# Performance work log

Hardware: AMD Instinct MI355X
Metric: run time of the kernel (lower is better)

## Reference

```python
import jax, jax.numpy as jnp
import numpy as np

N, K, D = 32768, 32, 64
LOG_2PI = float(np.log(2.0 * np.pi))


def setup_inputs() -> dict:
    key = jax.random.key(0)
    k1, k2, k3, k4 = jax.random.split(key, 4)
    X = jax.random.normal(k1, (N, D), dtype=jnp.float32)
    mu = jax.random.normal(k2, (K, D), dtype=jnp.float32)
    L = jax.random.normal(k3, (K, D, D), dtype=jnp.float32) * 0.1
    weights = jax.random.normal(k4, (K,), dtype=jnp.float32)
    return {"X": X, "mu": mu, "L": L, "weights": weights, "it": 0}


def reference(X, mu, L, weights, it):
    d = X.shape[1]
    # Cholesky composition: Sigma_k = tril(L_k) @ tril(L_k).T + I  (always PD)
    Lt = jnp.tril(L)                                   # [K, D, D]
    sigmas = Lt @ jnp.swapaxes(Lt, -1, -2) + jnp.eye(d, dtype=X.dtype)
    _, logdet = jnp.linalg.slogdet(sigmas)             # [K] (det > 0, sign = +1)
    Sinv = jnp.linalg.inv(sigmas)                      # [K, D, D]
    # Batched squared Mahalanobis distance: [N, K]
    diff = X[:, None, :] - mu[None, :, :]              # [N, K, D]
    maha = jnp.einsum("nkd,kde,nke->nk", diff, Sinv, diff)
    log_w = jax.nn.log_softmax(weights)                # [K]
    # log component density + log mixture weight
    logp = -0.5 * (d * LOG_2PI + logdet[None, :] + maha) + log_w[None, :]
    # pdf = sum_k exp(logp); log_likelihood = log(pdf)  (stable via logsumexp)
    loglik = jax.scipy.special.logsumexp(logp, axis=1)  # [N]
    # forward = -log_likelihoods(X).logsumexp(dim=0)
    return -jax.scipy.special.logsumexp(loglik, axis=0)
```

## Files before the change

kernel.cpp:

```cpp
#include <hip/hip_runtime.h>
#include <math.h>

#define DIM 64
#define KC 32
#define NPTS 32768
#define LOG_2PI 1.8378770664093453f
#define C0 (-58.0f)
#define ST 68

typedef __attribute__((ext_vector_type(8))) short short8;
typedef __attribute__((ext_vector_type(4))) float float4v;

__device__ __forceinline__ unsigned short f2bf(float f) {
    unsigned u = __float_as_uint(f);
    u += 0x7FFFu + ((u >> 16) & 1u);
    return (unsigned short)(u >> 16);
}

__device__ __forceinline__ float rdlane(float v, int l) {
    return __int_as_float(__builtin_amdgcn_readlane(__float_as_int(v), l));
}

template <int CTRL>
__device__ __forceinline__ float dpp_add(float x) {
    int t = __builtin_amdgcn_mov_dpp(__float_as_int(x), CTRL, 0xF, 0xF, true);
    return x + __int_as_float(t);
}
__device__ __forceinline__ float sum16(float x) {
    x = dpp_add<0xB1>(x);
    x = dpp_add<0x4E>(x);
    x = dpp_add<0x141>(x);
    x = dpp_add<0x140>(x);
    return x;
}

__global__ __launch_bounds__(256) void prep_kernel(
    const float* __restrict__ L, const float* __restrict__ mu,
    const float* __restrict__ w, short* __restrict__ Bpack,
    float* __restrict__ cstC)
{
    const int k = blockIdx.x;
    const int t = threadIdx.x;
    const int wv = t >> 6;
    const int ln = t & 63;
    __shared__ float Llds[DIM * ST];
    __shared__ float Sig[DIM * ST];
    __shared__ float Clds[DIM * ST];
    __shared__ float Ylds[DIM * ST];
    __shared__ float qlds[DIM];
    __shared__ float rdbuf[DIM];
    __shared__ float ldet;

    for (int idx = t; idx < DIM * DIM; idx += 256) {
        int r = idx >> 6, c = idx & 63;
        float v = L[(size_t)k * DIM * DIM + idx];
        Llds[r * ST + c] = (c <= r) ? v : 0.f;
    }
    for (int idx = t; idx < DIM * ST; idx += 256) {
        Clds[idx] = 0.f;
        Ylds[idx] = 0.f;
    }
    __syncthreads();

    {
        float Lr[DIM];
        const float2* lp = (const float2*)(Llds + ln * ST);
#pragma unroll
        for (int p = 0; p < 32; ++p) {
            float2 v = lp[p];
            Lr[2 * p] = v.x; Lr[2 * p + 1] = v.y;
        }
#pragma unroll 1
        for (int jj = 0; jj < 16; ++jj) {
            const int j = wv * 16 + jj;
            const float2* up = (const float2*)(Llds + j * ST);
            float a0 = 0.f, a1 = 0.f, a2 = 0.f, a3 = 0.f;
#pragma unroll
            for (int p = 0; p < 32; p += 2) {
                float2 u0 = up[p], u1 = up[p + 1];
                a0 = fmaf(Lr[2 * p], u0.x, a0);
                a1 = fmaf(Lr[2 * p + 1], u0.y, a1);
                a2 = fmaf(Lr[2 * p + 2], u1.x, a2);
                a3 = fmaf(Lr[2 * p + 3], u1.y, a3);
            }
            float s = (a0 + a1) + (a2 + a3);
            if (j == ln) s += 1.f;
            Sig[ln * ST + j] = s;
        }
    }
    __syncthreads();

    {
        const float2* crow = (const float2*)(Clds + ln * ST);
        const float2* yrow = (const float2*)(Ylds + ln * ST);
        float ld2 = 0.f;
#pragma unroll 1
        for (int c = 0; c < DIM; c += 4) {
            const float2* u0 = (const float2*)(Clds + (c + 0) * ST);
            const float2* u1 = (const float2*)(Clds + (c + 1) * ST);
            const float2* u2 = (const float2*)(Clds + (c + 2) * ST);
            const float2* u3 = (const float2*)(Clds + (c + 3) * ST);
            float si0 = 0.f, si1 = 0.f, si2 = 0.f, si3 = 0.f;
            if (wv == 0) {
                float d0a = 0.f, d0b = 0.f, d1a = 0.f, d1b = 0.f;
                float d2a = 0.f, d2b = 0.f, d3a = 0.f, d3b = 0.f;
#pragma unroll
                for (int p = 0; p < 32; ++p) {
                    float2 cr = crow[p];
                    float2 a0 = u0[p], a1 = u1[p], a2 = u2[p], a3 = u3[p];
                    d0a = fmaf(cr.x, a0.x, d0a); d0b = fmaf(cr.y, a0.y, d0b);
                    d1a = fmaf(cr.x, a1.x, d1a); d1b = fmaf(cr.y, a1.y, d1b);
                    d2a = fmaf(cr.x, a2.x, d2a); d2b = fmaf(cr.y, a2.y, d2b);
                    d3a = fmaf(cr.x, a3.x, d3a); d3b = fmaf(cr.y, a3.y, d3b);
                }
                const float4 sg = *(const float4*)(Sig + ln * ST + c);
                float s0 = sg.x - (d0a + d0b);
                float s1 = sg.y - (d1a + d1b);
                float s2 = sg.z - (d2a + d2b);
                float s3 = sg.w - (d3a + d3b);
                float dd0 = rdlane(s0, c + 0);
                float rd0 = __builtin_amdgcn_rsqf(dd0);
                float c0v = s0 * rd0;
                s1 = fmaf(-c0v, rdlane(c0v, c + 1), s1);
                s2 = fmaf(-c0v, rdlane(c0v, c + 2), s2);
                s3 = fmaf(-c0v, rdlane(c0v, c + 3), s3);
                float dd1 = rdlane(s1, c + 1);
                float rd1 = __builtin_amdgcn_rsqf(dd1);
                float c1v = s1 * rd1;
                s2 = fmaf(-c1v, rdlane(c1v, c + 2), s2);
                s3 = fmaf(-c1v, rdlane(c1v, c + 3), s3);
                float dd2 = rdlane(s2, c + 2);
                float rd2 = __builtin_amdgcn_rsqf(dd2);
                float c2v = s2 * rd2;
                s3 = fmaf(-c2v, rdlane(c2v, c + 3), s3);
                float dd3 = rdlane(s3, c + 3);
                float rd3 = __builtin_amdgcn_rsqf(dd3);
                float c3v = s3 * rd3;
                ld2 += (__logf(dd0) + __logf(dd1)) + (__logf(dd2) + __logf(dd3));
                *(float4*)(Clds + ln * ST + c) = make_float4(c0v, c1v, c2v, c3v);
                if (ln == 0) *(float4*)(rdbuf + c) = make_float4(rd0, rd1, rd2, rd3);
            } else if (wv == 1) {
                float e0a = 0.f, e0b = 0.f, e1a = 0.f, e1b = 0.f;
                float e2a = 0.f, e2b = 0.f, e3a = 0.f, e3b = 0.f;
#pragma unroll
                for (int p = 0; p < 32; ++p) {
                    float2 yr = yrow[p];
                    float2 a0 = u0[p], a1 = u1[p], a2 = u2[p], a3 = u3[p];
                    e0a = fmaf(yr.x, a0.x, e0a); e0b = fmaf(yr.y, a0.y, e0b);
                    e1a = fmaf(yr.x, a1.x, e1a); e1b = fmaf(yr.y, a1.y, e1b);
                    e2a = fmaf(yr.x, a2.x, e2a); e2b = fmaf(yr.y, a2.y, e2b);
                    e3a = fmaf(yr.x, a3.x, e3a); e3b = fmaf(yr.y, a3.y, e3b);
                }
                si0 = ((ln == c + 0) ? 1.f : 0.f) - (e0a + e0b);
                si1 = ((ln == c + 1) ? 1.f : 0.f) - (e1a + e1b);
                si2 = ((ln == c + 2) ? 1.f : 0.f) - (e2a + e2b);
                si3 = ((ln == c + 3) ? 1.f : 0.f) - (e3a + e3b);
            }
            __syncthreads();
            if (wv == 1) {
                const float4 rdv = *(const float4*)(rdbuf + c);
                float C10 = Clds[(c + 1) * ST + c];
                float C20 = Clds[(c + 2) * ST + c];
                float C21 = Clds[(c + 2) * ST + c + 1];
                float C30 = Clds[(c + 3) * ST + c];
                float C31 = Clds[(c + 3) * ST + c + 1];
                float C32 = Clds[(c + 3) * ST + c + 2];
                float y0 = si0 * rdv.x;
                float y1 = (si1 - C10 * y0) * rdv.y;
                float y2 = (si2 - C20 * y0 - C21 * y1) * rdv.z;
                float y3 = (si3 - C30 * y0 - C31 * y1 - C32 * y2) * rdv.w;
                float4 yo;
                yo.x = (ln <= c + 0) ? y0 : 0.f;
                yo.y = (ln <= c + 1) ? y1 : 0.f;
                yo.z = (ln <= c + 2) ? y2 : 0.f;
                yo.w = (ln <= c + 3) ? y3 : 0.f;
                *(float4*)(Ylds + ln * ST + c) = yo;
            }
        }
        if (wv == 0 && ln == 0) ldet = ld2;
    }
    __syncthreads();

    if (wv == 0) {
        const float* muk = mu + k * DIM;
        float qv = 0.f;
#pragma unroll 8
        for (int j = 0; j < DIM; ++j)
            qv = fmaf(Ylds[j * ST + ln], muk[j], qv);
        qlds[ln] = qv;
        if (ln == 0) {
            float wm = -3.0e38f;
            for (int i = 0; i < KC; ++i) wm = fmaxf(wm, w[i]);
            float se = 0.f;
            for (int i = 0; i < KC; ++i) se += __expf(w[i] - wm);
            float logw = w[k] - (wm + __logf(se));
            cstC[k] = -0.5f * (DIM * LOG_2PI + ldet) + logw - C0;
        }
    }
    __syncthreads();

    {
        const int ct = wv;
        const int col = ct * 16 + (ln & 15);
        const int kb = (ln >> 4) * 8;
#pragma unroll
        for (int kt = 0; kt < 3; ++kt) {
            short8 v;
            if (kt < 2) {
#pragma unroll
                for (int e = 0; e < 8; ++e)
                    v[e] = (short)f2bf(Ylds[(kt * 32 + kb + e) * ST + col]);
            } else {
#pragma unroll
                for (int e = 0; e < 8; ++e)
                    v[e] = (short)((kb + e == 0) ? f2bf(-qlds[col]) : 0);
            }
            *(short8*)(Bpack + ((size_t)(k * 12 + ct * 3 + kt) * 64 + ln) * 8) = v;
        }
    }
}

__global__ __launch_bounds__(256, 2) void main_kernel(
    const float* __restrict__ X, const float* __restrict__ Bpack,
    const float* __restrict__ cstC, float* __restrict__ partials)
{
    const int tid = threadIdx.x;
    const int lane = tid & 63;
    const int wv = tid >> 6;
    const int ks = blockIdx.x & 7;
    const int g = blockIdx.x >> 3;
    const int m = lane & 15;

    __shared__ float4 Bsh[3072];
    {
        const float4* Bg = (const float4*)Bpack + (size_t)ks * 3072;
#pragma unroll
        for (int it = 0; it < 12; ++it)
            Bsh[it * 256 + tid] = Bg[it * 256 + tid];
    }

    const int rbase = g * 128 + wv * 32;
    const int jb = (lane >> 4) * 8;
    const float* Xr0 = X + (size_t)(rbase + m) * DIM;
    const float* Xr1 = Xr0 + 16 * DIM;
    short8 a0, a1, b0r, b1r;
#pragma unroll
    for (int e = 0; e < 8; ++e) {
        a0[e] = (short)f2bf(Xr0[jb + e]);
        a1[e] = (short)f2bf(Xr0[32 + jb + e]);
        b0r[e] = (short)f2bf(Xr1[jb + e]);
        b1r[e] = (short)f2bf(Xr1[32 + jb + e]);
    }

    __syncthreads();

    const short8* Bs = (const short8*)Bsh;
    const short* Bss = (const short*)Bsh;
    float acc = 0.f;
#pragma unroll
    for (int kk = 0; kk < 4; ++kk) {
        const int k = ks * 4 + kk;
        float p0 = 0.f, p1 = 0.f, p2 = 0.f, p3 = 0.f;
        float r0 = 0.f, r1 = 0.f, r2 = 0.f, r3 = 0.f;
#pragma unroll
        for (int ct = 0; ct < 4; ++ct) {
            short8 f0 = Bs[(kk * 12 + ct * 3 + 0) * 64 + lane];
            short8 f1 = Bs[(kk * 12 + ct * 3 + 1) * 64 + lane];
            short nqs = Bss[(size_t)((kk * 12 + ct * 3 + 2) * 64 + m) * 8];
            float nq = __int_as_float(((int)(unsigned short)nqs) << 16);
            float4v c0 = {nq, nq, nq, nq};
            c0 = __builtin_amdgcn_mfma_f32_16x16x32_bf16(a0, f0, c0, 0, 0, 0);
            c0 = __builtin_amdgcn_mfma_f32_16x16x32_bf16(a1, f1, c0, 0, 0, 0);
            float4v c1 = {nq, nq, nq, nq};
            c1 = __builtin_amdgcn_mfma_f32_16x16x32_bf16(b0r, f0, c1, 0, 0, 0);
            c1 = __builtin_amdgcn_mfma_f32_16x16x32_bf16(b1r, f1, c1, 0, 0, 0);
            p0 = fmaf(c0[0], c0[0], p0); p1 = fmaf(c0[1], c0[1], p1);
            p2 = fmaf(c0[2], c0[2], p2); p3 = fmaf(c0[3], c0[3], p3);
            r0 = fmaf(c1[0], c1[0], r0); r1 = fmaf(c1[1], c1[1], r1);
            r2 = fmaf(c1[2], c1[2], r2); r3 = fmaf(c1[3], c1[3], r3);
        }
        const float cc = cstC[k];
        acc += __expf(fmaf(-0.5f, sum16(p0), cc)) + __expf(fmaf(-0.5f, sum16(p1), cc));
        acc += __expf(fmaf(-0.5f, sum16(p2), cc)) + __expf(fmaf(-0.5f, sum16(p3), cc));
        acc += __expf(fmaf(-0.5f, sum16(r0), cc)) + __expf(fmaf(-0.5f, sum16(r1), cc));
        acc += __expf(fmaf(-0.5f, sum16(r2), cc)) + __expf(fmaf(-0.5f, sum16(r3), cc));
    }
    acc += __shfl_xor(acc, 16, 64);
    acc += __shfl_xor(acc, 32, 64);

    __shared__ float pm[4];
    if (lane == 0) pm[wv] = acc;
    __syncthreads();
    if (tid == 0)
        partials[blockIdx.x] = (pm[0] + pm[1]) + (pm[2] + pm[3]);
}

__global__ __launch_bounds__(256) void final_kernel(
    const float* __restrict__ partials, int n, float* __restrict__ out)
{
    const int tid = threadIdx.x;
    float s = 0.f;
    for (int i = tid; i < n; i += 256) s += partials[i];
#pragma unroll
    for (int mm = 1; mm <= 32; mm <<= 1) s += __shfl_xor(s, mm, 64);
    __shared__ float pm[4];
    if ((tid & 63) == 0) pm[tid >> 6] = s;
    __syncthreads();
    if (tid == 0) out[0] = -(C0 + logf((pm[0] + pm[1]) + (pm[2] + pm[3])));
}

extern "C" void kernel_launch(void* const* d_in, const int* in_sizes, int n_in,
                              void* d_out, int out_size, void* d_ws, size_t ws_size,
                              hipStream_t stream) {
    const float* X  = (const float*)d_in[0];
    const float* mu = (const float*)d_in[1];
    const float* L  = (const float*)d_in[2];
    const float* w  = (const float*)d_in[3];

    char* ws = (char*)d_ws;
    short* Bpack = (short*)ws;
    float* cstC  = (float*)(ws + 32 * 12 * 64 * 8 * 2);
    float* parts = cstC + KC;

    prep_kernel<<<KC, 256, 0, stream>>>(L, mu, w, Bpack, cstC);
    main_kernel<<<2048, 256, 0, stream>>>(X, (const float*)Bpack, cstC, parts);
    final_kernel<<<1, 256, 0, stream>>>(parts, 2048, (float*)d_out);
}
```

Baseline: 113.3 us.

## Fuse prep, main and final reduction into one kernel with flag sync

Merges the per-component Cholesky/inverse prep, the MFMA Mahalanobis main pass and the final logsumexp into a single launch. The first 32 blocks do the prep work and publish ready flags; every block loads its X fragment first, then spins on the flags before staging the packed B matrices. The last block to finish, found through an atomic counter, performs the final reduction. This removes two kernel launches and lets X loads overlap the prep. The risks: the flags are never reset between calls, so later calls can read Bpack while it is being rewritten. Also, the larger shared-memory union and the spin-wait depend on the prep blocks being resident first.

```diff
diff --git a/kernel.cpp b/kernel.cpp
--- a/kernel.cpp
+++ b/kernel.cpp
@@ -7,6 +7,7 @@
 #define LOG_2PI 1.8378770664093453f
 #define C0 (-58.0f)
 #define ST 68
+#define MAGIC 0x13579BDF
 
 typedef __attribute__((ext_vector_type(8))) short short8;
 typedef __attribute__((ext_vector_type(4))) float float4v;
@@ -34,210 +35,221 @@
     return x;
 }
 
-__global__ __launch_bounds__(256) void prep_kernel(
-    const float* __restrict__ L, const float* __restrict__ mu,
-    const float* __restrict__ w, short* __restrict__ Bpack,
-    float* __restrict__ cstC)
+struct PrepSh {
+    float Llds[DIM * ST];
+    float Sig[DIM * ST];
+    float Clds[DIM * ST];
+    float Ylds[DIM * ST];
+    float qlds[DIM];
+    float rdbuf[DIM];
+    float ldet;
+};
+struct MainSh {
+    float4 Bsh[3072];
+    float pm[4];
+};
+union SharedU { PrepSh p; MainSh m; };
+
+__global__ __launch_bounds__(256, 2) void fused_kernel(
+    const float* __restrict__ X, const float* __restrict__ mu,
+    const float* __restrict__ L, const float* __restrict__ w,
+    short* __restrict__ Bpack, float* __restrict__ cstC,
+    float* __restrict__ partials, int* __restrict__ flags,
+    int* __restrict__ tailctr, float* __restrict__ out)
 {
-    const int k = blockIdx.x;
-    const int t = threadIdx.x;
-    const int wv = t >> 6;
-    const int ln = t & 63;
-    __shared__ float Llds[DIM * ST];
-    __shared__ float Sig[DIM * ST];
-    __shared__ float Clds[DIM * ST];
-    __shared__ float Ylds[DIM * ST];
-    __shared__ float qlds[DIM];
-    __shared__ float rdbuf[DIM];
-    __shared__ float ldet;
-
-    for (int idx = t; idx < DIM * DIM; idx += 256) {
-        int r = idx >> 6, c = idx & 63;
-        float v = L[(size_t)k * DIM * DIM + idx];
-        Llds[r * ST + c] = (c <= r) ? v : 0.f;
-    }
-    for (int idx = t; idx < DIM * ST; idx += 256) {
-        Clds[idx] = 0.f;
-        Ylds[idx] = 0.f;
-    }
-    __syncthreads();
-
-    {
-        float Lr[DIM];
-        const float2* lp = (const float2*)(Llds + ln * ST);
-#pragma unroll
-        for (int p = 0; p < 32; ++p) {
-            float2 v = lp[p];
-            Lr[2 * p] = v.x; Lr[2 * p + 1] = v.y;
-        }
-#pragma unroll 1
-        for (int jj = 0; jj < 16; ++jj) {
-            const int j = wv * 16 + jj;
-            const float2* up = (const float2*)(Llds + j * ST);
-            float a0 = 0.f, a1 = 0.f, a2 = 0.f, a3 = 0.f;
-#pragma unroll
-            for (int p = 0; p < 32; p += 2) {
-                float2 u0 = up[p], u1 = up[p + 1];
-                a0 = fmaf(Lr[2 * p], u0.x, a0);
-                a1 = fmaf(Lr[2 * p + 1], u0.y, a1);
-                a2 = fmaf(Lr[2 * p + 2], u1.x, a2);
-                a3 = fmaf(Lr[2 * p + 3], u1.y, a3);
-            }
-            float s = (a0 + a1) + (a2 + a3);
-            if (j == ln) s += 1.f;
-            Sig[ln * ST + j] = s;
-        }
-    }
-    __syncthreads();
-
-    {
-        const float2* crow = (const float2*)(Clds + ln * ST);
-        const float2* yrow = (const float2*)(Ylds + ln * ST);
-        float ld2 = 0.f;
-#pragma unroll 1
-        for (int c = 0; c < DIM; c += 4) {
-            const float2* u0 = (const float2*)(Clds + (c + 0) * ST);
-            const float2* u1 = (const float2*)(Clds + (c + 1) * ST);
-            const float2* u2 = (const float2*)(Clds + (c + 2) * ST);
-            const float2* u3 = (const float2*)(Clds + (c + 3) * ST);
-            float si0 = 0.f, si1 = 0.f, si2 = 0.f, si3 = 0.f;
-            if (wv == 0) {
-                float d0a = 0.f, d0b = 0.f, d1a = 0.f, d1b = 0.f;
-                float d2a = 0.f, d2b = 0.f, d3a = 0.f, d3b = 0.f;
-#pragma unroll
-                for (int p = 0; p < 32; ++p) {
-                    float2 cr = crow[p];
-                    float2 a0 = u0[p], a1 = u1[p], a2 = u2[p], a3 = u3[p];
-                    d0a = fmaf(cr.x, a0.x, d0a); d0b = fmaf(cr.y, a0.y, d0b);
-                    d1a = fmaf(cr.x, a1.x, d1a); d1b = fmaf(cr.y, a1.y, d1b);
-                    d2a = fmaf(cr.x, a2.x, d2a); d2b = fmaf(cr.y, a2.y, d2b);
-                    d3a = fmaf(cr.x, a3.x, d3a); d3b = fmaf(cr.y, a3.y, d3b);
-                }
-                const float4 sg = *(const float4*)(Sig + ln * ST + c);
-                float s0 = sg.x - (d0a + d0b);
-                float s1 = sg.y - (d1a + d1b);
-                float s2 = sg.z - (d2a + d2b);
-                float s3 = sg.w - (d3a + d3b);
-                float dd0 = rdlane(s0, c + 0);
-                float rd0 = __builtin_amdgcn_rsqf(dd0);
-                float c0v = s0 * rd0;
-                s1 = fmaf(-c0v, rdlane(c0v, c + 1), s1);
-                s2 = fmaf(-c0v, rdlane(c0v, c + 2), s2);
-                s3 = fmaf(-c0v, rdlane(c0v, c + 3), s3);
-                float dd1 = rdlane(s1, c + 1);
-                float rd1 = __builtin_amdgcn_rsqf(dd1);
-                float c1v = s1 * rd1;
-                s2 = fmaf(-c1v, rdlane(c1v, c + 2), s2);
-                s3 = fmaf(-c1v, rdlane(c1v, c + 3), s3);
-                float dd2 = rdlane(s2, c + 2);
-                float rd2 = __builtin_amdgcn_rsqf(dd2);
-                float c2v = s2 * rd2;
-                s3 = fmaf(-c2v, rdlane(c2v, c + 3), s3);
-                float dd3 = rdlane(s3, c + 3);
-                float rd3 = __builtin_amdgcn_rsqf(dd3);
-                float c3v = s3 * rd3;
-                ld2 += (__logf(dd0) + __logf(dd1)) + (__logf(dd2) + __logf(dd3));
-                *(float4*)(Clds + ln * ST + c) = make_float4(c0v, c1v, c2v, c3v);
-                if (ln == 0) *(float4*)(rdbuf + c) = make_float4(rd0, rd1, rd2, rd3);
-            } else if (wv == 1) {
-                float e0a = 0.f, e0b = 0.f, e1a = 0.f, e1b = 0.f;
-                float e2a = 0.f, e2b = 0.f, e3a = 0.f, e3b = 0.f;
-#pragma unroll
-                for (int p = 0; p < 32; ++p) {
-                    float2 yr = yrow[p];
-                    float2 a0 = u0[p], a1 = u1[p], a2 = u2[p], a3 = u3[p];
-                    e0a = fmaf(yr.x, a0.x, e0a); e0b = fmaf(yr.y, a0.y, e0b);
-                    e1a = fmaf(yr.x, a1.x, e1a); e1b = fmaf(yr.y, a1.y, e1b);
-                    e2a = fmaf(yr.x, a2.x, e2a); e2b = fmaf(yr.y, a2.y, e2b);
-                    e3a = fmaf(yr.x, a3.x, e3a); e3b = fmaf(yr.y, a3.y, e3b);
-                }
-                si0 = ((ln == c + 0) ? 1.f : 0.f) - (e0a + e0b);
-                si1 = ((ln == c + 1) ? 1.f : 0.f) - (e1a + e1b);
-                si2 = ((ln == c + 2) ? 1.f : 0.f) - (e2a + e2b);
-                si3 = ((ln == c + 3) ? 1.f : 0.f) - (e3a + e3b);
-            }
-            __syncthreads();
-            if (wv == 1) {
-                const float4 rdv = *(const float4*)(rdbuf + c);
-                float C10 = Clds[(c + 1) * ST + c];
-                float C20 = Clds[(c + 2) * ST + c];
-                float C21 = Clds[(c + 2) * ST + c + 1];
-                float C30 = Clds[(c + 3) * ST + c];
-                float C31 = Clds[(c + 3) * ST + c + 1];
-                float C32 = Clds[(c + 3) * ST + c + 2];
-                float y0 = si0 * rdv.x;
-                float y1 = (si1 - C10 * y0) * rdv.y;
-                float y2 = (si2 - C20 * y0 - C21 * y1) * rdv.z;
-                float y3 = (si3 - C30 * y0 - C31 * y1 - C32 * y2) * rdv.w;
-                float4 yo;
-                yo.x = (ln <= c + 0) ? y0 : 0.f;
-                yo.y = (ln <= c + 1) ? y1 : 0.f;
-                yo.z = (ln <= c + 2) ? y2 : 0.f;
-                yo.w = (ln <= c + 3) ? y3 : 0.f;
-                *(float4*)(Ylds + ln * ST + c) = yo;
-            }
-        }
-        if (wv == 0 && ln == 0) ldet = ld2;
-    }
-    __syncthreads();
-
-    if (wv == 0) {
-        const float* muk = mu + k * DIM;
-        float qv = 0.f;
-#pragma unroll 8
-        for (int j = 0; j < DIM; ++j)
-            qv = fmaf(Ylds[j * ST + ln], muk[j], qv);
-        qlds[ln] = qv;
-        if (ln == 0) {
-            float wm = -3.0e38f;
-            for (int i = 0; i < KC; ++i) wm = fmaxf(wm, w[i]);
-            float se = 0.f;
-            for (int i = 0; i < KC; ++i) se += __expf(w[i] - wm);
-            float logw = w[k] - (wm + __logf(se));
-            cstC[k] = -0.5f * (DIM * LOG_2PI + ldet) + logw - C0;
-        }
-    }
-    __syncthreads();
-
-    {
-        const int ct = wv;
-        const int col = ct * 16 + (ln & 15);
-        const int kb = (ln >> 4) * 8;
-#pragma unroll
-        for (int kt = 0; kt < 3; ++kt) {
-            short8 v;
-            if (kt < 2) {
-#pragma unroll
-                for (int e = 0; e < 8; ++e)
-                    v[e] = (short)f2bf(Ylds[(kt * 32 + kb + e) * ST + col]);
-            } else {
-#pragma unroll
-                for (int e = 0; e < 8; ++e)
-                    v[e] = (short)((kb + e == 0) ? f2bf(-qlds[col]) : 0);
-            }
-            *(short8*)(Bpack + ((size_t)(k * 12 + ct * 3 + kt) * 64 + ln) * 8) = v;
-        }
-    }
-}
-
-__global__ __launch_bounds__(256, 2) void main_kernel(
-    const float* __restrict__ X, const float* __restrict__ Bpack,
-    const float* __restrict__ cstC, float* __restrict__ partials)
-{
+    const int bid = blockIdx.x;
     const int tid = threadIdx.x;
     const int lane = tid & 63;
     const int wv = tid >> 6;
-    const int ks = blockIdx.x & 7;
-    const int g = blockIdx.x >> 3;
+    __shared__ SharedU sh;
+    __shared__ int lastdone;
+
+    if (bid == 0 && tid == 0) *tailctr = 0;
+
+    if (bid < KC) {
+        const int k = bid;
+        const int t = tid;
+        const int ln = lane;
+        float* Llds = sh.p.Llds;
+        float* Sig  = sh.p.Sig;
+        float* Clds = sh.p.Clds;
+        float* Ylds = sh.p.Ylds;
+
+        for (int idx = t; idx < DIM * DIM; idx += 256) {
+            int r = idx >> 6, c = idx & 63;
+            float v = L[(size_t)k * DIM * DIM + idx];
+            Llds[r * ST + c] = (c <= r) ? v : 0.f;
+        }
+        for (int idx = t; idx < DIM * ST; idx += 256) {
+            Clds[idx] = 0.f;
+            Ylds[idx] = 0.f;
+        }
+        __syncthreads();
+
+        {
+            float Lr[DIM];
+            const float2* lp = (const float2*)(Llds + ln * ST);
+#pragma unroll
+            for (int p = 0; p < 32; ++p) {
+                float2 v = lp[p];
+                Lr[2 * p] = v.x; Lr[2 * p + 1] = v.y;
+            }
+#pragma unroll 1
+            for (int jj = 0; jj < 16; ++jj) {
+                const int j = wv * 16 + jj;
+                const float2* up = (const float2*)(Llds + j * ST);
+                float a0 = 0.f, a1 = 0.f, a2 = 0.f, a3 = 0.f;
+#pragma unroll
+                for (int p = 0; p < 32; p += 2) {
+                    float2 u0 = up[p], u1 = up[p + 1];
+                    a0 = fmaf(Lr[2 * p], u0.x, a0);
+                    a1 = fmaf(Lr[2 * p + 1], u0.y, a1);
+                    a2 = fmaf(Lr[2 * p + 2], u1.x, a2);
+                    a3 = fmaf(Lr[2 * p + 3], u1.y, a3);
+                }
+                float s = (a0 + a1) + (a2 + a3);
+                if (j == ln) s += 1.f;
+                Sig[ln * ST + j] = s;
+            }
+        }
+        __syncthreads();
+
+        {
+            const float2* crow = (const float2*)(Clds + ln * ST);
+            const float2* yrow = (const float2*)(Ylds + ln * ST);
+            float ld2 = 0.f;
+#pragma unroll 1
+            for (int c = 0; c < DIM; c += 4) {
+                const float2* u0 = (const float2*)(Clds + (c + 0) * ST);
+                const float2* u1 = (const float2*)(Clds + (c + 1) * ST);
+                const float2* u2 = (const float2*)(Clds + (c + 2) * ST);
+                const float2* u3 = (const float2*)(Clds + (c + 3) * ST);
+                float si0 = 0.f, si1 = 0.f, si2 = 0.f, si3 = 0.f;
+                if (wv == 0) {
+                    float d0a = 0.f, d0b = 0.f, d1a = 0.f, d1b = 0.f;
+                    float d2a = 0.f, d2b = 0.f, d3a = 0.f, d3b = 0.f;
+#pragma unroll
+                    for (int p = 0; p < 32; ++p) {
+                        float2 cr = crow[p];
+                        float2 a0 = u0[p], a1 = u1[p], a2 = u2[p], a3 = u3[p];
+                        d0a = fmaf(cr.x, a0.x, d0a); d0b = fmaf(cr.y, a0.y, d0b);
+                        d1a = fmaf(cr.x, a1.x, d1a); d1b = fmaf(cr.y, a1.y, d1b);
+                        d2a = fmaf(cr.x, a2.x, d2a); d2b = fmaf(cr.y, a2.y, d2b);
+                        d3a = fmaf(cr.x, a3.x, d3a); d3b = fmaf(cr.y, a3.y, d3b);
+                    }
+                    const float4 sg = *(const float4*)(Sig + ln * ST + c);
+                    float s0 = sg.x - (d0a + d0b);
+                    float s1 = sg.y - (d1a + d1b);
+                    float s2 = sg.z - (d2a + d2b);
+                    float s3 = sg.w - (d3a + d3b);
+                    float dd0 = rdlane(s0, c + 0);
+                    float rd0 = __builtin_amdgcn_rsqf(dd0);
+                    float c0v = s0 * rd0;
+                    s1 = fmaf(-c0v, rdlane(c0v, c + 1), s1);
+                    s2 = fmaf(-c0v, rdlane(c0v, c + 2), s2);
+                    s3 = fmaf(-c0v, rdlane(c0v, c + 3), s3);
+                    float dd1 = rdlane(s1, c + 1);
+                    float rd1 = __builtin_amdgcn_rsqf(dd1);
+                    float c1v = s1 * rd1;
+                    s2 = fmaf(-c1v, rdlane(c1v, c + 2), s2);
+                    s3 = fmaf(-c1v, rdlane(c1v, c + 3), s3);
+                    float dd2 = rdlane(s2, c + 2);
+                    float rd2 = __builtin_amdgcn_rsqf(dd2);
+                    float c2v = s2 * rd2;
+                    s3 = fmaf(-c2v, rdlane(c2v, c + 3), s3);
+                    float dd3 = rdlane(s3, c + 3);
+                    float rd3 = __builtin_amdgcn_rsqf(dd3);
+                    float c3v = s3 * rd3;
+                    ld2 += (__logf(dd0) + __logf(dd1)) + (__logf(dd2) + __logf(dd3));
+                    *(float4*)(Clds + ln * ST + c) = make_float4(c0v, c1v, c2v, c3v);
+                    if (ln == 0) *(float4*)(sh.p.rdbuf + c) = make_float4(rd0, rd1, rd2, rd3);
+                } else if (wv == 1) {
+                    float e0a = 0.f, e0b = 0.f, e1a = 0.f, e1b = 0.f;
+                    float e2a = 0.f, e2b = 0.f, e3a = 0.f, e3b = 0.f;
+#pragma unroll
+                    for (int p = 0; p < 32; ++p) {
+                        float2 yr = yrow[p];
+                        float2 a0 = u0[p], a1 = u1[p], a2 = u2[p], a3 = u3[p];
+                        e0a = fmaf(yr.x, a0.x, e0a); e0b = fmaf(yr.y, a0.y, e0b);
+                        e1a = fmaf(yr.x, a1.x, e1a); e1b = fmaf(yr.y, a1.y, e1b);
+                        e2a = fmaf(yr.x, a2.x, e2a); e2b = fmaf(yr.y, a2.y, e2b);
+                        e3a = fmaf(yr.x, a3.x, e3a); e3b = fmaf(yr.y, a3.y, e3b);
+                    }
+                    si0 = ((ln == c + 0) ? 1.f : 0.f) - (e0a + e0b);
+                    si1 = ((ln == c + 1) ? 1.f : 0.f) - (e1a + e1b);
+                    si2 = ((ln == c + 2) ? 1.f : 0.f) - (e2a + e2b);
+                    si3 = ((ln == c + 3) ? 1.f : 0.f) - (e3a + e3b);
+                }
+                __syncthreads();
+                if (wv == 1) {
+                    const float4 rdv = *(const float4*)(sh.p.rdbuf + c);
+                    float C10 = Clds[(c + 1) * ST + c];
+                    float C20 = Clds[(c + 2) * ST + c];
+                    float C21 = Clds[(c + 2) * ST + c + 1];
+                    float C30 = Clds[(c + 3) * ST + c];
+                    float C31 = Clds[(c + 3) * ST + c + 1];
+                    float C32 = Clds[(c + 3) * ST + c + 2];
+                    float y0 = si0 * rdv.x;
+                    float y1 = (si1 - C10 * y0) * rdv.y;
+                    float y2 = (si2 - C20 * y0 - C21 * y1) * rdv.z;
+                    float y3 = (si3 - C30 * y0 - C31 * y1 - C32 * y2) * rdv.w;
+                    float4 yo;
+                    yo.x = (ln <= c + 0) ? y0 : 0.f;
+                    yo.y = (ln <= c + 1) ? y1 : 0.f;
+                    yo.z = (ln <= c + 2) ? y2 : 0.f;
+                    yo.w = (ln <= c + 3) ? y3 : 0.f;
+                    *(float4*)(Ylds + ln * ST + c) = yo;
+                }
+            }
+            if (wv == 0 && ln == 0) sh.p.ldet = ld2;
+        }
+        __syncthreads();
+
+        if (wv == 0) {
+            const float* muk = mu + k * DIM;
+            float qv = 0.f;
+#pragma unroll 8
+            for (int j = 0; j < DIM; ++j)
+                qv = fmaf(Ylds[j * ST + ln], muk[j], qv);
+            sh.p.qlds[ln] = qv;
+            if (ln == 0) {
+                float wm = -3.0e38f;
+                for (int i = 0; i < KC; ++i) wm = fmaxf(wm, w[i]);
+                float se = 0.f;
+                for (int i = 0; i < KC; ++i) se += __expf(w[i] - wm);
+                float logw = w[k] - (wm + __logf(se));
+                cstC[k] = -0.5f * (DIM * LOG_2PI + sh.p.ldet) + logw - C0;
+            }
+        }
+        __syncthreads();
+
+        {
+            const int ct = wv;
+            const int col = ct * 16 + (ln & 15);
+            const int kb = (ln >> 4) * 8;
+#pragma unroll
+            for (int kt = 0; kt < 3; ++kt) {
+                short8 v;
+                if (kt < 2) {
+#pragma unroll
+                    for (int e = 0; e < 8; ++e)
+                        v[e] = (short)f2bf(Ylds[(kt * 32 + kb + e) * ST + col]);
+                } else {
+#pragma unroll
+                    for (int e = 0; e < 8; ++e)
+                        v[e] = (short)((kb + e == 0) ? f2bf(-sh.p.qlds[col]) : 0);
+                }
+                *(short8*)(Bpack + ((size_t)(k * 12 + ct * 3 + kt) * 64 + ln) * 8) = v;
+            }
+        }
+        __threadfence();
+        __syncthreads();
+        if (tid == 0) atomicExch(&flags[k], MAGIC);
+    }
+
+    const int ks = bid & 7;
+    const int g = bid >> 3;
     const int m = lane & 15;
-
-    __shared__ float4 Bsh[3072];
-    {
-        const float4* Bg = (const float4*)Bpack + (size_t)ks * 3072;
-#pragma unroll
-        for (int it = 0; it < 12; ++it)
-            Bsh[it * 256 + tid] = Bg[it * 256 + tid];
-    }
 
     const int rbase = g * 128 + wv * 32;
     const int jb = (lane >> 4) * 8;
@@ -252,10 +264,23 @@
         b1r[e] = (short)f2bf(Xr1[32 + jb + e]);
     }
 
+    if (tid < KC) {
+        while (__hip_atomic_load(&flags[tid], __ATOMIC_ACQUIRE,
+                                 __HIP_MEMORY_SCOPE_AGENT) != MAGIC)
+            __builtin_amdgcn_s_sleep(2);
+    }
     __syncthreads();
 
-    const short8* Bs = (const short8*)Bsh;
-    const short* Bss = (const short*)Bsh;
+    {
+        const float4* Bg = (const float4*)Bpack + (size_t)ks * 3072;
+#pragma unroll
+        for (int it = 0; it < 12; ++it)
+            sh.m.Bsh[it * 256 + tid] = Bg[it * 256 + tid];
+    }
+    __syncthreads();
+
+    const short8* Bs = (const short8*)sh.m.Bsh;
+    const short* Bss = (const short*)sh.m.Bsh;
     float acc = 0.f;
 #pragma unroll
     for (int kk = 0; kk < 4; ++kk) {
@@ -288,25 +313,24 @@
     acc += __shfl_xor(acc, 16, 64);
     acc += __shfl_xor(acc, 32, 64);
 
-    __shared__ float pm[4];
-    if (lane == 0) pm[wv] = acc;
+    if (lane == 0) sh.m.pm[wv] = acc;
     __syncthreads();
-    if (tid == 0)
-        partials[blockIdx.x] = (pm[0] + pm[1]) + (pm[2] + pm[3]);
-}
-
-__global__ __launch_bounds__(256) void final_kernel(
-    const float* __restrict__ partials, int n, float* __restrict__ out)
-{
-    const int tid = threadIdx.x;
-    float s = 0.f;
-    for (int i = tid; i < n; i += 256) s += partials[i];
-#pragma unroll
-    for (int mm = 1; mm <= 32; mm <<= 1) s += __shfl_xor(s, mm, 64);
-    __shared__ float pm[4];
-    if ((tid & 63) == 0) pm[tid >> 6] = s;
+    if (tid == 0) {
+        partials[bid] = (sh.m.pm[0] + sh.m.pm[1]) + (sh.m.pm[2] + sh.m.pm[3]);
+        __threadfence();
+        lastdone = (atomicAdd(tailctr, 1) == 2047) ? 1 : 0;
+    }
     __syncthreads();
-    if (tid == 0) out[0] = -(C0 + logf((pm[0] + pm[1]) + (pm[2] + pm[3])));
+    if (lastdone) {
+        __threadfence();
+        float s = 0.f;
+        for (int i = tid; i < 2048; i += 256) s += partials[i];
+#pragma unroll
+        for (int mm = 1; mm <= 32; mm <<= 1) s += __shfl_xor(s, mm, 64);
+        if (lane == 0) sh.m.pm[wv] = s;
+        __syncthreads();
+        if (tid == 0) out[0] = -(C0 + logf((sh.m.pm[0] + sh.m.pm[1]) + (sh.m.pm[2] + sh.m.pm[3])));
+    }
 }
 
 extern "C" void kernel_launch(void* const* d_in, const int* in_sizes, int n_in,
@@ -318,11 +342,12 @@
     const float* w  = (const float*)d_in[3];
 
     char* ws = (char*)d_ws;
-    short* Bpack = (short*)ws;
-    float* cstC  = (float*)(ws + 32 * 12 * 64 * 8 * 2);
-    float* parts = cstC + KC;
-
-    prep_kernel<<<KC, 256, 0, stream>>>(L, mu, w, Bpack, cstC);
-    main_kernel<<<2048, 256, 0, stream>>>(X, (const float*)Bpack, cstC, parts);
-    final_kernel<<<1, 256, 0, stream>>>(parts, 2048, (float*)d_out);
-}
+    short* Bpack   = (short*)ws;
+    float* cstC    = (float*)(ws + 32 * 12 * 64 * 8 * 2);
+    float* parts   = cstC + KC;
+    int*   flags   = (int*)(parts + 2048);
+    int*   tailctr = flags + KC;
+
+    fused_kernel<<<2048, 256, 0, stream>>>(X, mu, L, w, Bpack, cstC,
+                                           parts, flags, tailctr, (float*)d_out);
+}
```

Measured after the change: 194.8 us. 1.72x slower.
